# Kernel tuning notes

Hardware: AMD Instinct MI355X
Metric: run time of the kernel (lower is better)

Reference implementation:

```python
import jax, jax.numpy as jnp
import numpy as np

N, E, M = 50000, 50000, 640000
IN_DIM, D, L = 256, 128, 3

def setup_inputs() -> dict:
    key = jax.random.key(0)
    ks = jax.random.split(key, 8)
    x = jax.random.normal(ks[0], (N, IN_DIM), dtype=jnp.float32)
    hyperedge_index = jax.random.randint(ks[1], (2, M), 0, N, dtype=jnp.int64)
    weightMatrix = jax.random.uniform(ks[2], (E,), dtype=jnp.float32)
    edgesWeights = jax.random.uniform(ks[3], (M,), dtype=jnp.float32)
    stdv_fc = 1.0 / np.sqrt(IN_DIM)
    fc_w = jax.random.uniform(ks[4], (IN_DIM, D), minval=-stdv_fc, maxval=stdv_fc, dtype=jnp.float32)
    fc_b = jax.random.uniform(ks[5], (D,), minval=-stdv_fc, maxval=stdv_fc, dtype=jnp.float32)
    stdv = 1.0 / np.sqrt(D)
    conv_w = jax.random.uniform(ks[6], (L, D, D), minval=-stdv, maxval=stdv, dtype=jnp.float32)
    conv_b = jax.random.uniform(ks[7], (L, D), minval=-stdv, maxval=stdv, dtype=jnp.float32)
    return {"x": x, "hyperedge_index": hyperedge_index, "weightMatrix": weightMatrix,
            "edgesWeights": edgesWeights, "fc_w": fc_w, "fc_b": fc_b,
            "conv_w": conv_w, "conv_b": conv_b}

def reference(x, hyperedge_index, weightMatrix, edgesWeights, fc_w, fc_b, conv_w, conv_b):
    row, col = hyperedge_index[0], hyperedge_index[1]
    n_nodes, n_edges = x.shape[0], weightMatrix.shape[0]
    # degree normalization (computed once, shared by all layers since inputs identical)
    node_deg = jax.ops.segment_sum(weightMatrix[col], row, num_segments=n_nodes) + 1e-8
    hyper_deg = jax.ops.segment_sum(edgesWeights, col, num_segments=n_edges) + 1e-8
    nd = node_deg ** -0.5
    nd = jnp.where(jnp.isinf(nd), 0.0, nd)
    hd = hyper_deg ** -0.5
    hd = jnp.where(jnp.isinf(hd), 0.0, hd)
    norm = hd[col] * nd[row]  # [M]
    h = jax.nn.relu(x @ fc_w + fc_b)  # [N, D]; dropout inactive (eval)
    for i in range(conv_w.shape[0]):
        xt = h @ conv_w[i] + conv_b[i]                                  # [N, D]
        wx = xt[row] * (edgesWeights * norm)[:, None]                   # [M, D]
        hyper_feat = jax.ops.segment_sum(wx, col, num_segments=n_edges)  # [E, D]
        wh = hyper_feat[col] * (weightMatrix[col] * edgesWeights * norm)[:, None]  # [M, D]
        z = jax.ops.segment_sum(wh, row, num_segments=n_nodes)           # [N, D]
        h = jax.nn.relu(h + z)
    return h
```

## Files before the change

### kernel.cpp

```cpp
#include <hip/hip_runtime.h>
#include <hip/hip_bf16.h>
#include <stdint.h>

typedef __attribute__((ext_vector_type(4))) float f4;
typedef __attribute__((ext_vector_type(2))) float f2;
typedef __attribute__((ext_vector_type(2))) int i2;
typedef __attribute__((ext_vector_type(8))) unsigned short us8;
typedef __attribute__((ext_vector_type(4))) unsigned short us4;
typedef __attribute__((ext_vector_type(2))) unsigned short us2;
typedef __attribute__((ext_vector_type(8))) short s8b;
typedef __attribute__((ext_vector_type(4))) float f32x4;

#define CW_SHIFT 7
#define CH 2048

__device__ __forceinline__ float bf2f(unsigned short u) {
  union { unsigned int i; float f; } t; t.i = ((unsigned int)u) << 16; return t.f;
}
__device__ __forceinline__ unsigned short f2bf(float f) {
  union { float f; unsigned int i; } t; t.f = f;
  unsigned int u = t.i;
  return (unsigned short)((u + 0x7FFFu + ((u >> 16) & 1u)) >> 16);
}
__device__ __forceinline__ float cvtload(const void* p, int i, int f16) {
  return f16 ? bf2f(((const unsigned short*)p)[i]) : ((const float*)p)[i];
}

__global__ void detect_kernel(const unsigned int* __restrict__ xb,
                              const unsigned int* __restrict__ ib,
                              int* __restrict__ flags) {
  if (threadIdx.x == 0) {
    int cnt = 0;
    for (int i = 0; i < 256; ++i) {
      unsigned int e = (xb[i] >> 7) & 0xffu;
      if (e >= 110u && e <= 135u) ++cnt;
    }
    flags[0] = (cnt >= 180) ? 1 : 0;
    int zc = 0;
    for (int i = 0; i < 128; ++i) if (ib[2 * i + 1] == 0u) ++zc;
    flags[1] = (zc >= 120) ? 1 : 0;
  }
}

__global__ void cvt_params(const void* __restrict__ wM, const void* __restrict__ fcw,
                           const void* __restrict__ fcb, const void* __restrict__ cw,
                           const void* __restrict__ cb,
                           float* __restrict__ WMf, unsigned short* __restrict__ FCWT,
                           float* __restrict__ FCB, unsigned short* __restrict__ CWT,
                           float* __restrict__ CBf,
                           int E, int L, const int* __restrict__ flags) {
  const int IN_DIM = 256, D = 128;
  int i = blockIdx.x * 256 + threadIdx.x;
  const int f16 = flags[0];
  if (i < E) { WMf[i] = cvtload(wM, i, f16); return; }
  i -= E;
  if (i < IN_DIM * D) {
    int c = i >> 8, k = i & 255;
    FCWT[i] = f2bf(cvtload(fcw, k * D + c, f16));
    return;
  }
  i -= IN_DIM * D;
  if (i < D) { FCB[i] = cvtload(fcb, i, f16); return; }
  i -= D;
  if (i < L * D * D) {
    int l = i >> 14, rem = i & 16383;
    int c = rem >> 7, k = rem & 127;
    CWT[i] = f2bf(cvtload(cw, l * D * D + k * D + c, f16));
    return;
  }
  i -= L * D * D;
  if (i < L * D) CBf[i] = cvtload(cb, i, f16);
}

__global__ __launch_bounds__(256) void bin_count(
    const void* __restrict__ hei, int M, int* __restrict__ cntAB,
    int nbE, int nbN, int nblk, const int* __restrict__ flags) {
  __shared__ int hA[512];
  __shared__ int hB[512];
  const int tid = threadIdx.x, blk = blockIdx.x;
  for (int b = tid; b < 512; b += 256) { hA[b] = 0; hB[b] = 0; }
  __syncthreads();
  const int i64 = flags[1];
  const int mEnd = min(M, (blk + 1) * CH);
  for (int m = blk * CH + tid; m < mEnd; m += 256) {
    int r, c;
    if (i64) {
      r = (int)((const long long*)hei)[m];
      c = (int)((const long long*)hei)[M + m];
    } else {
      r = ((const int*)hei)[m];
      c = ((const int*)hei)[M + m];
    }
    atomicAdd(&hA[c >> CW_SHIFT], 1);
    atomicAdd(&hB[r >> CW_SHIFT], 1);
  }
  __syncthreads();
  for (int b = tid; b < nbE; b += 256) cntAB[b * nblk + blk] = hA[b];
  for (int b = tid; b < nbN; b += 256) cntAB[(nbE + b) * nblk + blk] = hB[b];
}

__global__ __launch_bounds__(512) void scanA(int* __restrict__ cnt,
                                             int* __restrict__ btot, int nblk) {
  __shared__ int sc[512];
  const int tid = threadIdx.x, b = blockIdx.x;
  int v = (tid < nblk) ? cnt[b * nblk + tid] : 0;
  sc[tid] = v;
  __syncthreads();
  for (int s = 1; s < 512; s <<= 1) {
    int t = (tid >= s) ? sc[tid - s] : 0;
    __syncthreads();
    sc[tid] += t;
    __syncthreads();
  }
  if (tid < nblk) cnt[b * nblk + tid] = sc[tid] - v;
  if (tid == 511) btot[b] = sc[511];
}

__global__ __launch_bounds__(512) void scanB(const int* __restrict__ btot,
                                             int* __restrict__ bbaseA,
                                             int* __restrict__ bbaseB,
                                             int nbE, int nbN) {
  __shared__ int sc[512];
  const int tid = threadIdx.x;
  const int nb = blockIdx.x ? nbN : nbE;
  const int* src = blockIdx.x ? (btot + nbE) : btot;
  int* dst = blockIdx.x ? bbaseB : bbaseA;
  int v = (tid < nb) ? src[tid] : 0;
  sc[tid] = v;
  __syncthreads();
  for (int s = 1; s < 512; s <<= 1) {
    int t = (tid >= s) ? sc[tid - s] : 0;
    __syncthreads();
    sc[tid] += t;
    __syncthreads();
  }
  if (tid < nb) dst[tid] = sc[tid] - v;
  if (tid == 511) dst[nb] = sc[511];
}

__global__ __launch_bounds__(256) void binscatter(
    const void* __restrict__ hei, const void* __restrict__ ew, int M,
    const int* __restrict__ cntAB,
    const int* __restrict__ bbaseA, const int* __restrict__ bbaseB,
    i2* __restrict__ PAYA, i2* __restrict__ PAYB,
    int nbE, int nbN, int nblk, const int* __restrict__ flags) {
  __shared__ int baseA[512];
  __shared__ int baseB[512];
  const int tid = threadIdx.x, blk = blockIdx.x;
  for (int b = tid; b < nbE; b += 256) baseA[b] = bbaseA[b] + cntAB[b * nblk + blk];
  for (int b = tid; b < nbN; b += 256) baseB[b] = bbaseB[b] + cntAB[(nbE + b) * nblk + blk];
  __syncthreads();
  const int i64 = flags[1], f16 = flags[0];
  const int mEnd = min(M, (blk + 1) * CH);
  for (int m = blk * CH + tid; m < mEnd; m += 256) {
    int r, c;
    if (i64) {
      r = (int)((const long long*)hei)[m];
      c = (int)((const long long*)hei)[M + m];
    } else {
      r = ((const int*)hei)[m];
      c = ((const int*)hei)[M + m];
    }
    int e = __float_as_int(f16 ? bf2f(((const unsigned short*)ew)[m])
                               : ((const float*)ew)[m]);
    int pA = atomicAdd(&baseA[c >> CW_SHIFT], 1);
    i2 ea; ea[0] = r | ((c & 127) << 20); ea[1] = e;
    PAYA[pA] = ea;
    int pB = atomicAdd(&baseB[r >> CW_SHIFT], 1);
    i2 eb; eb[0] = c | ((r & 127) << 20); eb[1] = e;
    PAYB[pB] = eb;
  }
}

__global__ __launch_bounds__(256) void finalize3(
    const i2* __restrict__ PAYA, const int* __restrict__ bbaseA,
    i2* __restrict__ ENTA, int* __restrict__ offE, int E,
    const i2* __restrict__ PAYB, const int* __restrict__ bbaseB,
    i2* __restrict__ ENTB, int* __restrict__ offN, int Nn,
    const float* __restrict__ WMf, float* __restrict__ SCE,
    float* __restrict__ ND, int nbE) {
  __shared__ int cnt[128];
  __shared__ int sc[128];
  __shared__ int cur[128];
  __shared__ float fsum[128];
  int b = blockIdx.x;
  const i2* PAY; const int* bbase; i2* ENT; int* off;
  int nseg, modeB; float* outScale;
  if (b < nbE) {
    PAY = PAYA; bbase = bbaseA; ENT = ENTA; off = offE;
    nseg = E; modeB = 0; outScale = SCE;
  } else {
    b -= nbE;
    PAY = PAYB; bbase = bbaseB; ENT = ENTB; off = offN;
    nseg = Nn; modeB = 1; outScale = ND;
  }
  const int tid = threadIdx.x;
  const int bs = bbase[b], be = bbase[b + 1];
  const int cb = b << CW_SHIFT;
  const int cw = min(128, nseg - cb);
  if (tid < 128) { cnt[tid] = 0; fsum[tid] = 0.f; }
  __syncthreads();
  for (int k = bs + tid; k < be; k += 256)
    atomicAdd(&cnt[(PAY[k][0] >> 20) & 127], 1);
  __syncthreads();
  if (tid < 128) sc[tid] = cnt[tid];
  __syncthreads();
  for (int s = 1; s < 128; s <<= 1) {
    int t = (tid < 128 && tid >= s) ? sc[tid - s] : 0;
    __syncthreads();
    if (tid < 128) sc[tid] += t;
    __syncthreads();
  }
  if (tid < 128) {
    int start = bs + sc[tid] - cnt[tid];
    cur[tid] = start;
    if (tid < cw) off[cb + tid] = start;
  }
  if (tid == 0 && b == ((nseg + 127) >> CW_SHIFT) - 1) off[nseg] = be;
  __syncthreads();
  for (int k = bs + tid; k < be; k += 256) {
    i2 p = PAY[k];
    int key = (p[0] >> 20) & 127;
    int src = p[0] & 0xFFFFF;
    int pos = atomicAdd(&cur[key], 1);
    i2 outp; outp[0] = src; outp[1] = p[1];
    ENT[pos] = outp;
    float add = modeB ? WMf[src] : __int_as_float(p[1]);
    atomicAdd(&fsum[key], add);
  }
  __syncthreads();
  if (tid < cw) {
    float s = fsum[tid] + 1e-8f;
    outScale[cb + tid] = modeB ? rsqrtf(s) : (WMf[cb + tid] / s);
  }
}

template<int KS>
__global__ __launch_bounds__(256) void gemm_mfma3(
    const void* __restrict__ Aptr, const unsigned short* __restrict__ Wt,
    const float* __restrict__ bias, unsigned short* __restrict__ out,
    int Nrows, const int* __restrict__ flags, int relu,
    const float* __restrict__ rowScale) {
  constexpr int K = KS * 32;
  constexpr int KC = K / 8;
  extern __shared__ unsigned short Bs[];
  const int tid = threadIdx.x;
  const int wv = tid >> 6, ln = tid & 63;
  const int lr = ln & 15;
  const int lk = (ln >> 4) << 3;
  const int rowBase = blockIdx.x * 128 + wv * 32;
  const int aF32 = flags ? (flags[0] ? 0 : 1) : 0;

  int ar[2];
#pragma unroll
  for (int t = 0; t < 2; ++t) {
    int r = rowBase + t * 16 + lr;
    ar[t] = (r < Nrows) ? r : (Nrows - 1);
  }

  s8b aR[2][KS];
  if (!aF32) {
#pragma unroll
    for (int t = 0; t < 2; ++t)
#pragma unroll
      for (int ks = 0; ks < KS; ++ks)
        aR[t][ks] = *reinterpret_cast<const s8b*>(
            (const unsigned short*)Aptr + (size_t)ar[t] * K + ks * 32 + lk);
  } else {
#pragma unroll
    for (int t = 0; t < 2; ++t)
#pragma unroll
      for (int ks = 0; ks < KS; ++ks) {
        const float* ap = (const float*)Aptr + (size_t)ar[t] * K + ks * 32 + lk;
        f4 u0 = *reinterpret_cast<const f4*>(ap);
        f4 u1 = *reinterpret_cast<const f4*>(ap + 4);
#pragma unroll
        for (int j = 0; j < 4; ++j) {
          aR[t][ks][j]     = (short)f2bf(u0[j]);
          aR[t][ks][4 + j] = (short)f2bf(u1[j]);
        }
      }
  }

#pragma unroll
  for (int it = 0; it < (128 * KC + 255) / 256; ++it) {
    int ch = it * 256 + tid;
    if (ch < 128 * KC) {
      int row = ch / KC, kc = (ch % KC) << 3;
      us8 v = *reinterpret_cast<const us8*>(Wt + (size_t)row * K + kc);
      int byte = ((row * K + kc) << 1) ^ ((row & 7) << 4);
      *reinterpret_cast<us8*>((char*)Bs + byte) = v;
    }
  }
  __syncthreads();

  f32x4 acc[2][8];
#pragma unroll
  for (int t = 0; t < 2; ++t)
#pragma unroll
    for (int n = 0; n < 8; ++n) acc[t][n] = (f32x4)0.f;

#pragma unroll
  for (int ks = 0; ks < KS; ++ks) {
#pragma unroll
    for (int n = 0; n < 8; ++n) {
      const int brow = n * 16 + lr;
      int byte = ((brow * K + ks * 32 + lk) << 1) ^ ((brow & 7) << 4);
      s8b b = *reinterpret_cast<const s8b*>((const char*)Bs + byte);
      acc[0][n] = __builtin_amdgcn_mfma_f32_16x16x32_bf16(aR[0][ks], b, acc[0][n], 0, 0, 0);
      acc[1][n] = __builtin_amdgcn_mfma_f32_16x16x32_bf16(aR[1][ks], b, acc[1][n], 0, 0, 0);
    }
  }

#pragma unroll
  for (int t = 0; t < 2; ++t) {
    const int orow0 = rowBase + t * 16 + ((ln >> 4) << 2);
#pragma unroll
    for (int n = 0; n < 8; ++n) {
      const int col = n * 16 + lr;
      const float bv = bias[col];
#pragma unroll
      for (int r = 0; r < 4; ++r) {
        int row = orow0 + r;
        if (row >= Nrows) continue;
        float s = acc[t][n][r] + bv;
        if (relu) s = fmaxf(s, 0.f);
        if (rowScale) s *= rowScale[row];
        out[(size_t)row * 128 + col] = f2bf(s);
      }
    }
  }
}

__global__ __launch_bounds__(256) void gather_edge3(
    const int* __restrict__ off, const i2* __restrict__ ENT,
    const float* __restrict__ sc_e, const unsigned short* __restrict__ X,
    unsigned short* __restrict__ out, int nseg) {
  int seg = blockIdx.x * 8 + (threadIdx.x >> 5);
  if (seg >= nseg) return;
  int d = (threadIdx.x & 31) << 2;
  int k0 = off[seg], k1 = off[seg + 1];
  float a0 = 0.f, a1 = 0.f, a2 = 0.f, a3 = 0.f;
  int k = k0;
  for (; k + 4 <= k1; k += 4) {
    i2 e0 = ENT[k], e1 = ENT[k + 1], e2 = ENT[k + 2], e3 = ENT[k + 3];
    us4 v0 = *reinterpret_cast<const us4*>(X + (size_t)e0[0] * 128 + d);
    us4 v1 = *reinterpret_cast<const us4*>(X + (size_t)e1[0] * 128 + d);
    us4 v2 = *reinterpret_cast<const us4*>(X + (size_t)e2[0] * 128 + d);
    us4 v3 = *reinterpret_cast<const us4*>(X + (size_t)e3[0] * 128 + d);
    float c0 = __int_as_float(e0[1]), c1 = __int_as_float(e1[1]);
    float c2 = __int_as_float(e2[1]), c3 = __int_as_float(e3[1]);
    a0 += c0 * bf2f(v0[0]); a1 += c0 * bf2f(v0[1]); a2 += c0 * bf2f(v0[2]); a3 += c0 * bf2f(v0[3]);
    a0 += c1 * bf2f(v1[0]); a1 += c1 * bf2f(v1[1]); a2 += c1 * bf2f(v1[2]); a3 += c1 * bf2f(v1[3]);
    a0 += c2 * bf2f(v2[0]); a1 += c2 * bf2f(v2[1]); a2 += c2 * bf2f(v2[2]); a3 += c2 * bf2f(v2[3]);
    a0 += c3 * bf2f(v3[0]); a1 += c3 * bf2f(v3[1]); a2 += c3 * bf2f(v3[2]); a3 += c3 * bf2f(v3[3]);
  }
  for (; k < k1; ++k) {
    i2 e = ENT[k];
    us4 v = *reinterpret_cast<const us4*>(X + (size_t)e[0] * 128 + d);
    float c = __int_as_float(e[1]);
    a0 += c * bf2f(v[0]); a1 += c * bf2f(v[1]); a2 += c * bf2f(v[2]); a3 += c * bf2f(v[3]);
  }
  float sc = sc_e[seg];
  us4 o;
  o[0] = f2bf(sc * a0); o[1] = f2bf(sc * a1); o[2] = f2bf(sc * a2); o[3] = f2bf(sc * a3);
  *reinterpret_cast<us4*>(out + (size_t)seg * 128 + d) = o;
}

__global__ __launch_bounds__(256) void gather_node3(
    const int* __restrict__ off, const i2* __restrict__ ENT,
    const float* __restrict__ nd, const unsigned short* __restrict__ HF,
    const unsigned short* __restrict__ H, void* __restrict__ out,
    int nseg, int outF32) {
  int seg = blockIdx.x * 8 + (threadIdx.x >> 5);
  if (seg >= nseg) return;
  int d = (threadIdx.x & 31) << 2;
  int k0 = off[seg], k1 = off[seg + 1];
  float a0 = 0.f, a1 = 0.f, a2 = 0.f, a3 = 0.f;
  int k = k0;
  for (; k + 4 <= k1; k += 4) {
    i2 e0 = ENT[k], e1 = ENT[k + 1], e2 = ENT[k + 2], e3 = ENT[k + 3];
    us4 v0 = *reinterpret_cast<const us4*>(HF + (size_t)e0[0] * 128 + d);
    us4 v1 = *reinterpret_cast<const us4*>(HF + (size_t)e1[0] * 128 + d);
    us4 v2 = *reinterpret_cast<const us4*>(HF + (size_t)e2[0] * 128 + d);
    us4 v3 = *reinterpret_cast<const us4*>(HF + (size_t)e3[0] * 128 + d);
    float c0 = __int_as_float(e0[1]), c1 = __int_as_float(e1[1]);
    float c2 = __int_as_float(e2[1]), c3 = __int_as_float(e3[1]);
    a0 += c0 * bf2f(v0[0]); a1 += c0 * bf2f(v0[1]); a2 += c0 * bf2f(v0[2]); a3 += c0 * bf2f(v0[3]);
    a0 += c1 * bf2f(v1[0]); a1 += c1 * bf2f(v1[1]); a2 += c1 * bf2f(v1[2]); a3 += c1 * bf2f(v1[3]);
    a0 += c2 * bf2f(v2[0]); a1 += c2 * bf2f(v2[1]); a2 += c2 * bf2f(v2[2]); a3 += c2 * bf2f(v2[3]);
    a0 += c3 * bf2f(v3[0]); a1 += c3 * bf2f(v3[1]); a2 += c3 * bf2f(v3[2]); a3 += c3 * bf2f(v3[3]);
  }
  for (; k < k1; ++k) {
    i2 e = ENT[k];
    us4 v = *reinterpret_cast<const us4*>(HF + (size_t)e[0] * 128 + d);
    float c = __int_as_float(e[1]);
    a0 += c * bf2f(v[0]); a1 += c * bf2f(v[1]); a2 += c * bf2f(v[2]); a3 += c * bf2f(v[3]);
  }
  float s = nd[seg];
  us4 h = *reinterpret_cast<const us4*>(H + (size_t)seg * 128 + d);
  float r0 = fmaxf(bf2f(h[0]) + s * a0, 0.f);
  float r1 = fmaxf(bf2f(h[1]) + s * a1, 0.f);
  float r2 = fmaxf(bf2f(h[2]) + s * a2, 0.f);
  float r3 = fmaxf(bf2f(h[3]) + s * a3, 0.f);
  if (outF32) {
    f4 o; o[0] = r0; o[1] = r1; o[2] = r2; o[3] = r3;
    *reinterpret_cast<f4*>((float*)out + (size_t)seg * 128 + d) = o;
  } else {
    us4 o; o[0] = f2bf(r0); o[1] = f2bf(r1); o[2] = f2bf(r2); o[3] = f2bf(r3);
    *reinterpret_cast<us4*>((unsigned short*)out + (size_t)seg * 128 + d) = o;
  }
}

extern "C" void kernel_launch(void* const* d_in, const int* in_sizes, int n_in,
                              void* d_out, int out_size, void* d_ws, size_t ws_size,
                              hipStream_t stream) {
  const void* x   = d_in[0];
  const void* hei = d_in[1];
  const void* wM  = d_in[2];
  const void* ew  = d_in[3];
  const void* fcw = d_in[4];
  const void* fcb = d_in[5];
  const void* cw  = d_in[6];
  const void* cb  = d_in[7];

  const int IN_DIM = 256, D = 128;
  const int N = in_sizes[0] / IN_DIM;
  const int M = in_sizes[1] / 2;
  const int E = in_sizes[2];
  const int L = in_sizes[6] / (D * D);

  const int nbE = (E + 127) >> CW_SHIFT;
  const int nbN = (N + 127) >> CW_SHIFT;
  const int nbT = nbE + nbN;
  const int nblk = (M + CH - 1) / CH;

  float* w = (float*)d_ws;
  size_t o = 0;
  auto alloc = [&](size_t n) { float* p = w + o; o += (n + 3) & ~(size_t)3; return p; };

  float* R = alloc((size_t)(N + E) * D / 2);
  unsigned short* XT = (unsigned short*)R;
  unsigned short* HF = XT + (size_t)N * D;
  i2*  PAYA = (i2*)R;
  i2*  PAYB = PAYA + M;

  unsigned short* H  = (unsigned short*)alloc((size_t)N * D / 2);
  i2*    ENTA = (i2*)alloc((size_t)M * 2);
  i2*    ENTB = (i2*)alloc((size_t)M * 2);
  int*   cntAB = (int*)alloc((size_t)nbT * nblk);
  int*   btotAB = (int*)alloc(nbT + 2);
  int*   bbaseA = (int*)alloc(nbE + 2);
  int*   bbaseB = (int*)alloc(nbN + 2);
  float* ND   = alloc(N);
  float* SCE  = alloc(E);
  int*   offE = (int*)alloc(E + 1);
  int*   offN = (int*)alloc(N + 1);
  float* WMf  = alloc(E);
  unsigned short* FCWT = (unsigned short*)alloc((size_t)IN_DIM * D / 2);
  float* FCB  = alloc(D);
  unsigned short* CWT = (unsigned short*)alloc((size_t)L * D * D / 2);
  float* CBf  = alloc((size_t)L * D);
  int*   FLAGS = (int*)alloc(16);

  detect_kernel<<<1, 64, 0, stream>>>((const unsigned int*)x, (const unsigned int*)hei, FLAGS);

  bin_count<<<nblk, 256, 0, stream>>>(hei, M, cntAB, nbE, nbN, nblk, FLAGS);
  {
    int ntot = E + IN_DIM * D + D + L * D * D + L * D;
    cvt_params<<<(ntot + 255) / 256, 256, 0, stream>>>(wM, fcw, fcb, cw, cb,
                                                       WMf, FCWT, FCB, CWT, CBf,
                                                       E, L, FLAGS);
  }

  scanA<<<nbT, 512, 0, stream>>>(cntAB, btotAB, nblk);
  scanB<<<2, 512, 0, stream>>>(btotAB, bbaseA, bbaseB, nbE, nbN);

  binscatter<<<nblk, 256, 0, stream>>>(hei, ew, M, cntAB, bbaseA, bbaseB,
                                       PAYA, PAYB, nbE, nbN, nblk, FLAGS);

  finalize3<<<nbT, 256, 0, stream>>>(PAYA, bbaseA, ENTA, offE, E,
                                     PAYB, bbaseB, ENTB, offN, N,
                                     WMf, SCE, ND, nbE);

  gemm_mfma3<8><<<(N + 127) / 128, 256, 128 * 256 * 2, stream>>>(
      x, FCWT, FCB, H, N, FLAGS, 1, nullptr);

  int segBlkE = (E + 7) / 8, segBlkN = (N + 7) / 8;
  for (int l = 0; l < L; ++l) {
    gemm_mfma3<4><<<(N + 127) / 128, 256, 128 * 128 * 2, stream>>>(
        H, CWT + (size_t)l * D * D, CBf + (size_t)l * D, XT, N,
        (const int*)nullptr, 0, ND);
    gather_edge3<<<segBlkE, 256, 0, stream>>>(offE, ENTA, SCE, XT, HF, E);
    gather_node3<<<segBlkN, 256, 0, stream>>>(
        offN, ENTB, ND, HF, H,
        (l == L - 1) ? d_out : (void*)H, N, (l == L - 1) ? 1 : 0);
  }
}
```

Measured before the change: 321.8 us.

## Use 16 lanes per segment with 16-byte gathers and widen CSR bins to 256

The edge and node gather kernels now give each segment 16 lanes, each loading eight bf16 values (16 bytes) per neighbour row instead of four. Each block therefore handles 16 segments rather than 8. Separately, the binning width for the CSR build grows from 128 to 256 segments per bin, which halves the number of bins and makes the finalize scan cover 256 entries. The wider loads are meant to cut gather instruction count and increase memory-level parallelism, at the cost of more registers per thread and fewer finalize blocks (lower parallelism in setup).

```diff
diff --git a/kernel.cpp b/kernel.cpp
--- a/kernel.cpp
+++ b/kernel.cpp
@@ -11,7 +11,8 @@
 typedef __attribute__((ext_vector_type(8))) short s8b;
 typedef __attribute__((ext_vector_type(4))) float f32x4;
 
-#define CW_SHIFT 7
+#define CW_SHIFT 8
+#define CW (1 << CW_SHIFT)
 #define CH 2048
 
 __device__ __forceinline__ float bf2f(unsigned short u) {
@@ -75,10 +76,10 @@
 __global__ __launch_bounds__(256) void bin_count(
     const void* __restrict__ hei, int M, int* __restrict__ cntAB,
     int nbE, int nbN, int nblk, const int* __restrict__ flags) {
-  __shared__ int hA[512];
-  __shared__ int hB[512];
+  __shared__ int hA[256];
+  __shared__ int hB[256];
   const int tid = threadIdx.x, blk = blockIdx.x;
-  for (int b = tid; b < 512; b += 256) { hA[b] = 0; hB[b] = 0; }
+  hA[tid] = 0; hB[tid] = 0;
   __syncthreads();
   const int i64 = flags[1];
   const int mEnd = min(M, (blk + 1) * CH);
@@ -95,8 +96,8 @@
     atomicAdd(&hB[r >> CW_SHIFT], 1);
   }
   __syncthreads();
-  for (int b = tid; b < nbE; b += 256) cntAB[b * nblk + blk] = hA[b];
-  for (int b = tid; b < nbN; b += 256) cntAB[(nbE + b) * nblk + blk] = hB[b];
+  if (tid < nbE) cntAB[tid * nblk + blk] = hA[tid];
+  if (tid < nbN) cntAB[(nbE + tid) * nblk + blk] = hB[tid];
 }
 
 __global__ __launch_bounds__(512) void scanA(int* __restrict__ cnt,
@@ -144,11 +145,11 @@
     const int* __restrict__ bbaseA, const int* __restrict__ bbaseB,
     i2* __restrict__ PAYA, i2* __restrict__ PAYB,
     int nbE, int nbN, int nblk, const int* __restrict__ flags) {
-  __shared__ int baseA[512];
-  __shared__ int baseB[512];
+  __shared__ int baseA[256];
+  __shared__ int baseB[256];
   const int tid = threadIdx.x, blk = blockIdx.x;
-  for (int b = tid; b < nbE; b += 256) baseA[b] = bbaseA[b] + cntAB[b * nblk + blk];
-  for (int b = tid; b < nbN; b += 256) baseB[b] = bbaseB[b] + cntAB[(nbE + b) * nblk + blk];
+  if (tid < nbE) baseA[tid] = bbaseA[tid] + cntAB[tid * nblk + blk];
+  if (tid < nbN) baseB[tid] = bbaseB[tid] + cntAB[(nbE + tid) * nblk + blk];
   __syncthreads();
   const int i64 = flags[1], f16 = flags[0];
   const int mEnd = min(M, (blk + 1) * CH);
@@ -164,10 +165,10 @@
     int e = __float_as_int(f16 ? bf2f(((const unsigned short*)ew)[m])
                                : ((const float*)ew)[m]);
     int pA = atomicAdd(&baseA[c >> CW_SHIFT], 1);
-    i2 ea; ea[0] = r | ((c & 127) << 20); ea[1] = e;
+    i2 ea; ea[0] = r | ((c & (CW - 1)) << 20); ea[1] = e;
     PAYA[pA] = ea;
     int pB = atomicAdd(&baseB[r >> CW_SHIFT], 1);
-    i2 eb; eb[0] = c | ((r & 127) << 20); eb[1] = e;
+    i2 eb; eb[0] = c | ((r & (CW - 1)) << 20); eb[1] = e;
     PAYB[pB] = eb;
   }
 }
@@ -179,10 +180,10 @@
     i2* __restrict__ ENTB, int* __restrict__ offN, int Nn,
     const float* __restrict__ WMf, float* __restrict__ SCE,
     float* __restrict__ ND, int nbE) {
-  __shared__ int cnt[128];
-  __shared__ int sc[128];
-  __shared__ int cur[128];
-  __shared__ float fsum[128];
+  __shared__ int cnt[CW];
+  __shared__ int sc[CW];
+  __shared__ int cur[CW];
+  __shared__ float fsum[CW];
   int b = blockIdx.x;
   const i2* PAY; const int* bbase; i2* ENT; int* off;
   int nseg, modeB; float* outScale;
@@ -197,30 +198,30 @@
   const int tid = threadIdx.x;
   const int bs = bbase[b], be = bbase[b + 1];
   const int cb = b << CW_SHIFT;
-  const int cw = min(128, nseg - cb);
-  if (tid < 128) { cnt[tid] = 0; fsum[tid] = 0.f; }
+  const int cw = min(CW, nseg - cb);
+  for (int i = tid; i < CW; i += 256) { cnt[i] = 0; fsum[i] = 0.f; }
   __syncthreads();
   for (int k = bs + tid; k < be; k += 256)
-    atomicAdd(&cnt[(PAY[k][0] >> 20) & 127], 1);
-  __syncthreads();
-  if (tid < 128) sc[tid] = cnt[tid];
-  __syncthreads();
-  for (int s = 1; s < 128; s <<= 1) {
-    int t = (tid < 128 && tid >= s) ? sc[tid - s] : 0;
+    atomicAdd(&cnt[(PAY[k][0] >> 20) & (CW - 1)], 1);
+  __syncthreads();
+  for (int i = tid; i < CW; i += 256) sc[i] = cnt[i];
+  __syncthreads();
+  for (int s = 1; s < CW; s <<= 1) {
+    int t = (tid >= s) ? sc[tid - s] : 0;
     __syncthreads();
-    if (tid < 128) sc[tid] += t;
+    sc[tid] += t;
     __syncthreads();
   }
-  if (tid < 128) {
+  {
     int start = bs + sc[tid] - cnt[tid];
     cur[tid] = start;
     if (tid < cw) off[cb + tid] = start;
   }
-  if (tid == 0 && b == ((nseg + 127) >> CW_SHIFT) - 1) off[nseg] = be;
+  if (tid == 0 && b == ((nseg + CW - 1) >> CW_SHIFT) - 1) off[nseg] = be;
   __syncthreads();
   for (int k = bs + tid; k < be; k += 256) {
     i2 p = PAY[k];
-    int key = (p[0] >> 20) & 127;
+    int key = (p[0] >> 20) & (CW - 1);
     int src = p[0] & 0xFFFFF;
     int pos = atomicAdd(&cur[key], 1);
     i2 outp; outp[0] = src; outp[1] = p[1];
@@ -336,35 +337,41 @@
     const int* __restrict__ off, const i2* __restrict__ ENT,
     const float* __restrict__ sc_e, const unsigned short* __restrict__ X,
     unsigned short* __restrict__ out, int nseg) {
-  int seg = blockIdx.x * 8 + (threadIdx.x >> 5);
+  int seg = blockIdx.x * 16 + (threadIdx.x >> 4);
   if (seg >= nseg) return;
-  int d = (threadIdx.x & 31) << 2;
+  int d = (threadIdx.x & 15) << 3;
   int k0 = off[seg], k1 = off[seg + 1];
-  float a0 = 0.f, a1 = 0.f, a2 = 0.f, a3 = 0.f;
+  float a0 = 0.f, a1 = 0.f, a2 = 0.f, a3 = 0.f, a4 = 0.f, a5 = 0.f, a6 = 0.f, a7 = 0.f;
   int k = k0;
   for (; k + 4 <= k1; k += 4) {
     i2 e0 = ENT[k], e1 = ENT[k + 1], e2 = ENT[k + 2], e3 = ENT[k + 3];
-    us4 v0 = *reinterpret_cast<const us4*>(X + (size_t)e0[0] * 128 + d);
-    us4 v1 = *reinterpret_cast<const us4*>(X + (size_t)e1[0] * 128 + d);
-    us4 v2 = *reinterpret_cast<const us4*>(X + (size_t)e2[0] * 128 + d);
-    us4 v3 = *reinterpret_cast<const us4*>(X + (size_t)e3[0] * 128 + d);
+    us8 v0 = *reinterpret_cast<const us8*>(X + (size_t)e0[0] * 128 + d);
+    us8 v1 = *reinterpret_cast<const us8*>(X + (size_t)e1[0] * 128 + d);
+    us8 v2 = *reinterpret_cast<const us8*>(X + (size_t)e2[0] * 128 + d);
+    us8 v3 = *reinterpret_cast<const us8*>(X + (size_t)e3[0] * 128 + d);
     float c0 = __int_as_float(e0[1]), c1 = __int_as_float(e1[1]);
     float c2 = __int_as_float(e2[1]), c3 = __int_as_float(e3[1]);
     a0 += c0 * bf2f(v0[0]); a1 += c0 * bf2f(v0[1]); a2 += c0 * bf2f(v0[2]); a3 += c0 * bf2f(v0[3]);
+    a4 += c0 * bf2f(v0[4]); a5 += c0 * bf2f(v0[5]); a6 += c0 * bf2f(v0[6]); a7 += c0 * bf2f(v0[7]);
     a0 += c1 * bf2f(v1[0]); a1 += c1 * bf2f(v1[1]); a2 += c1 * bf2f(v1[2]); a3 += c1 * bf2f(v1[3]);
+    a4 += c1 * bf2f(v1[4]); a5 += c1 * bf2f(v1[5]); a6 += c1 * bf2f(v1[6]); a7 += c1 * bf2f(v1[7]);
     a0 += c2 * bf2f(v2[0]); a1 += c2 * bf2f(v2[1]); a2 += c2 * bf2f(v2[2]); a3 += c2 * bf2f(v2[3]);
+    a4 += c2 * bf2f(v2[4]); a5 += c2 * bf2f(v2[5]); a6 += c2 * bf2f(v2[6]); a7 += c2 * bf2f(v2[7]);
     a0 += c3 * bf2f(v3[0]); a1 += c3 * bf2f(v3[1]); a2 += c3 * bf2f(v3[2]); a3 += c3 * bf2f(v3[3]);
+    a4 += c3 * bf2f(v3[4]); a5 += c3 * bf2f(v3[5]); a6 += c3 * bf2f(v3[6]); a7 += c3 * bf2f(v3[7]);
   }
   for (; k < k1; ++k) {
     i2 e = ENT[k];
-    us4 v = *reinterpret_cast<const us4*>(X + (size_t)e[0] * 128 + d);
+    us8 v = *reinterpret_cast<const us8*>(X + (size_t)e[0] * 128 + d);
     float c = __int_as_float(e[1]);
     a0 += c * bf2f(v[0]); a1 += c * bf2f(v[1]); a2 += c * bf2f(v[2]); a3 += c * bf2f(v[3]);
+    a4 += c * bf2f(v[4]); a5 += c * bf2f(v[5]); a6 += c * bf2f(v[6]); a7 += c * bf2f(v[7]);
   }
   float sc = sc_e[seg];
-  us4 o;
+  us8 o;
   o[0] = f2bf(sc * a0); o[1] = f2bf(sc * a1); o[2] = f2bf(sc * a2); o[3] = f2bf(sc * a3);
-  *reinterpret_cast<us4*>(out + (size_t)seg * 128 + d) = o;
+  o[4] = f2bf(sc * a4); o[5] = f2bf(sc * a5); o[6] = f2bf(sc * a6); o[7] = f2bf(sc * a7);
+  *reinterpret_cast<us8*>(out + (size_t)seg * 128 + d) = o;
 }
 
 __global__ __launch_bounds__(256) void gather_node3(
@@ -372,43 +379,58 @@
     const float* __restrict__ nd, const unsigned short* __restrict__ HF,
     const unsigned short* __restrict__ H, void* __restrict__ out,
     int nseg, int outF32) {
-  int seg = blockIdx.x * 8 + (threadIdx.x >> 5);
+  int seg = blockIdx.x * 16 + (threadIdx.x >> 4);
   if (seg >= nseg) return;
-  int d = (threadIdx.x & 31) << 2;
+  int d = (threadIdx.x & 15) << 3;
   int k0 = off[seg], k1 = off[seg + 1];
-  float a0 = 0.f, a1 = 0.f, a2 = 0.f, a3 = 0.f;
+  float a0 = 0.f, a1 = 0.f, a2 = 0.f, a3 = 0.f, a4 = 0.f, a5 = 0.f, a6 = 0.f, a7 = 0.f;
   int k = k0;
   for (; k + 4 <= k1; k += 4) {
     i2 e0 = ENT[k], e1 = ENT[k + 1], e2 = ENT[k + 2], e3 = ENT[k + 3];
-    us4 v0 = *reinterpret_cast<const us4*>(HF + (size_t)e0[0] * 128 + d);
-    us4 v1 = *reinterpret_cast<const us4*>(HF + (size_t)e1[0] * 128 + d);
-    us4 v2 = *reinterpret_cast<const us4*>(HF + (size_t)e2[0] * 128 + d);
-    us4 v3 = *reinterpret_cast<const us4*>(HF + (size_t)e3[0] * 128 + d);
+    us8 v0 = *reinterpret_cast<const us8*>(HF + (size_t)e0[0] * 128 + d);
+    us8 v1 = *reinterpret_cast<const us8*>(HF + (size_t)e1[0] * 128 + d);
+    us8 v2 = *reinterpret_cast<const us8*>(HF + (size_t)e2[0] * 128 + d);
+    us8 v3 = *reinterpret_cast<const us8*>(HF + (size_t)e3[0] * 128 + d);
     float c0 = __int_as_float(e0[1]), c1 = __int_as_float(e1[1]);
     float c2 = __int_as_float(e2[1]), c3 = __int_as_float(e3[1]);
     a0 += c0 * bf2f(v0[0]); a1 += c0 * bf2f(v0[1]); a2 += c0 * bf2f(v0[2]); a3 += c0 * bf2f(v0[3]);
+    a4 += c0 * bf2f(v0[4]); a5 += c0 * bf2f(v0[5]); a6 += c0 * bf2f(v0[6]); a7 += c0 * bf2f(v0[7]);
     a0 += c1 * bf2f(v1[0]); a1 += c1 * bf2f(v1[1]); a2 += c1 * bf2f(v1[2]); a3 += c1 * bf2f(v1[3]);
+    a4 += c1 * bf2f(v1[4]); a5 += c1 * bf2f(v1[5]); a6 += c1 * bf2f(v1[6]); a7 += c1 * bf2f(v1[7]);
     a0 += c2 * bf2f(v2[0]); a1 += c2 * bf2f(v2[1]); a2 += c2 * bf2f(v2[2]); a3 += c2 * bf2f(v2[3]);
+    a4 += c2 * bf2f(v2[4]); a5 += c2 * bf2f(v2[5]); a6 += c2 * bf2f(v2[6]); a7 += c2 * bf2f(v2[7]);
     a0 += c3 * bf2f(v3[0]); a1 += c3 * bf2f(v3[1]); a2 += c3 * bf2f(v3[2]); a3 += c3 * bf2f(v3[3]);
+    a4 += c3 * bf2f(v3[4]); a5 += c3 * bf2f(v3[5]); a6 += c3 * bf2f(v3[6]); a7 += c3 * bf2f(v3[7]);
   }
   for (; k < k1; ++k) {
     i2 e = ENT[k];
-    us4 v = *reinterpret_cast<const us4*>(HF + (size_t)e[0] * 128 + d);
+    us8 v = *reinterpret_cast<const us8*>(HF + (size_t)e[0] * 128 + d);
     float c = __int_as_float(e[1]);
     a0 += c * bf2f(v[0]); a1 += c * bf2f(v[1]); a2 += c * bf2f(v[2]); a3 += c * bf2f(v[3]);
+    a4 += c * bf2f(v[4]); a5 += c * bf2f(v[5]); a6 += c * bf2f(v[6]); a7 += c * bf2f(v[7]);
   }
   float s = nd[seg];
-  us4 h = *reinterpret_cast<const us4*>(H + (size_t)seg * 128 + d);
+  us8 h = *reinterpret_cast<const us8*>(H + (size_t)seg * 128 + d);
   float r0 = fmaxf(bf2f(h[0]) + s * a0, 0.f);
   float r1 = fmaxf(bf2f(h[1]) + s * a1, 0.f);
   float r2 = fmaxf(bf2f(h[2]) + s * a2, 0.f);
   float r3 = fmaxf(bf2f(h[3]) + s * a3, 0.f);
+  float r4 = fmaxf(bf2f(h[4]) + s * a4, 0.f);
+  float r5 = fmaxf(bf2f(h[5]) + s * a5, 0.f);
+  float r6 = fmaxf(bf2f(h[6]) + s * a6, 0.f);
+  float r7 = fmaxf(bf2f(h[7]) + s * a7, 0.f);
   if (outF32) {
-    f4 o; o[0] = r0; o[1] = r1; o[2] = r2; o[3] = r3;
-    *reinterpret_cast<f4*>((float*)out + (size_t)seg * 128 + d) = o;
+    float* op = (float*)out + (size_t)seg * 128 + d;
+    f4 o0, o1;
+    o0[0] = r0; o0[1] = r1; o0[2] = r2; o0[3] = r3;
+    o1[0] = r4; o1[1] = r5; o1[2] = r6; o1[3] = r7;
+    *reinterpret_cast<f4*>(op) = o0;
+    *reinterpret_cast<f4*>(op + 4) = o1;
   } else {
-    us4 o; o[0] = f2bf(r0); o[1] = f2bf(r1); o[2] = f2bf(r2); o[3] = f2bf(r3);
-    *reinterpret_cast<us4*>((unsigned short*)out + (size_t)seg * 128 + d) = o;
+    us8 o;
+    o[0] = f2bf(r0); o[1] = f2bf(r1); o[2] = f2bf(r2); o[3] = f2bf(r3);
+    o[4] = f2bf(r4); o[5] = f2bf(r5); o[6] = f2bf(r6); o[7] = f2bf(r7);
+    *reinterpret_cast<us8*>((unsigned short*)out + (size_t)seg * 128 + d) = o;
   }
 }
 
@@ -430,8 +452,8 @@
   const int E = in_sizes[2];
   const int L = in_sizes[6] / (D * D);
 
-  const int nbE = (E + 127) >> CW_SHIFT;
-  const int nbN = (N + 127) >> CW_SHIFT;
+  const int nbE = (E + CW - 1) >> CW_SHIFT;
+  const int nbN = (N + CW - 1) >> CW_SHIFT;
   const int nbT = nbE + nbN;
   const int nblk = (M + CH - 1) / CH;
 
@@ -486,7 +508,7 @@
   gemm_mfma3<8><<<(N + 127) / 128, 256, 128 * 256 * 2, stream>>>(
       x, FCWT, FCB, H, N, FLAGS, 1, nullptr);
 
-  int segBlkE = (E + 7) / 8, segBlkN = (N + 7) / 8;
+  int segBlkE = (E + 15) / 16, segBlkN = (N + 15) / 16;
   for (int l = 0; l < L; ++l) {
     gemm_mfma3<4><<<(N + 127) / 128, 256, 128 * 128 * 2, stream>>>(
         H, CWT + (size_t)l * D * D, CBf + (size_t)l * D, XT, N,
```

Result: faster. 307.5 us (-4.4%).
